# Optimization experiments

Measured on AMD Instinct MI355X. Metric: run time of the kernel, lower is better.

The kernel has to match this reference:

```python
import jax, jax.numpy as jnp
import numpy as np

T, F_IN, UNITS, N_CLASSES = 21, 126, 8, 27


def _run_lstm(seq, Wk, Wr, b):
    """Keras-style LSTM (gate order i,f,g,o). seq: (B,T,F) -> hs: (B,T,U)."""
    B = seq.shape[0]
    U = Wr.shape[0]
    # input projection for all timesteps at once: (B,T,4U)
    z_in = jnp.einsum('btf,fg->btg', seq, Wk) + b

    def step(carry, z_t):
        h, c = carry
        z = z_t + h @ Wr
        i, f, g, o = jnp.split(z, 4, axis=-1)
        i = jax.nn.sigmoid(i)
        f = jax.nn.sigmoid(f)
        g = jnp.tanh(g)
        o = jax.nn.sigmoid(o)
        c = f * c + i * g
        h = o * jnp.tanh(c)
        return (h, c), h

    h0 = jnp.zeros((B, U), seq.dtype)
    (_, _), hs = jax.lax.scan(step, (h0, h0), jnp.swapaxes(z_in, 0, 1))
    return jnp.swapaxes(hs, 0, 1)  # (B,T,U)


def setup_inputs() -> dict:
    key = jax.random.key(0)
    ks = jax.random.split(key, 6)
    B = 32768
    return {
        'x': jax.random.normal(ks[0], (B, T * F_IN), dtype=jnp.float32),
        'W1k': jax.random.normal(ks[1], (F_IN, 4 * UNITS), dtype=jnp.float32) * 0.1,
        'W1r': jax.random.normal(ks[2], (UNITS, 4 * UNITS), dtype=jnp.float32) * 0.1,
        'b1': jnp.zeros((4 * UNITS,), jnp.float32),
        'W2k': jax.random.normal(ks[3], (UNITS, 4 * UNITS), dtype=jnp.float32) * 0.1,
        'W2r': jax.random.normal(ks[4], (UNITS, 4 * UNITS), dtype=jnp.float32) * 0.1,
        'b2': jnp.zeros((4 * UNITS,), jnp.float32),
        'Wd': jax.random.normal(ks[5], (UNITS, N_CLASSES), dtype=jnp.float32) * 0.1,
        'bd': jnp.zeros((N_CLASSES,), jnp.float32),
    }


def reference(x, W1k, W1r, b1, W2k, W2r, b2, Wd, bd):
    B = x.shape[0]
    seq = x.reshape(B, T, F_IN)            # Reshape((21, 126))
    h1 = _run_lstm(seq, W1k, W1r, b1)      # LSTM(8, return_sequences=True)
    # dropout is identity at inference
    h2 = _run_lstm(h1, W2k, W2r, b2)[:, -1]  # LSTM(8) -> last step (B,8)
    return jax.nn.softmax(h2 @ Wd + bd)    # Dense(27, softmax)
```

## Files before the change

kernel.cpp:

```cpp
#include <hip/hip_runtime.h>


namespace {
constexpr int T_  = 21;
constexpr int FIN = 126;
constexpr int U_  = 8;
constexpr int NC  = 27;
constexpr int ZC  = 4 * U_;
constexpr int ROW = T_ * FIN;
constexpr size_t ZGRP = (size_t)T_ * ZC * 64;
}

__device__ __forceinline__ float sigm(float x) {
  return __builtin_amdgcn_rcpf(1.0f + __expf(-x));
}
__device__ __forceinline__ float tanh_f(float x) {
  return 1.0f - 2.0f * __builtin_amdgcn_rcpf(1.0f + __expf(2.0f * x));
}

__global__ __launch_bounds__(256) void zin_gemm(
    const float* __restrict__ X, const float* __restrict__ W1k,
    const float* __restrict__ b1, float* __restrict__ Z,
    int g0)
{
  __shared__ __align__(16) float xbuf[64 * FIN];

  const int tid = threadIdx.x;
  const int sl  = tid & 63;
  const int wv  = __builtin_amdgcn_readfirstlane(tid >> 6);
  const int grp = g0 + blockIdx.x;
  const int t   = blockIdx.y;

  const float* xbase = X + (size_t)grp * 64 * ROW + t * FIN;
  #pragma unroll
  for (int k = 0; k < 16; ++k) {
    int j = tid + k * 256;
    if (j < 64 * 63) {
      int s = j / 63;
      int q = j - s * 63;
      float2 v = *reinterpret_cast<const float2*>(xbase + (size_t)s * ROW + 2 * q);
      *reinterpret_cast<float2*>(&xbuf[s * FIN + 2 * q]) = v;
    }
  }
  __syncthreads();

  const float4* Wk4 = reinterpret_cast<const float4*>(W1k) + 2 * wv;
  float4 za = reinterpret_cast<const float4*>(b1)[2 * wv];
  float4 zb = reinterpret_cast<const float4*>(b1)[2 * wv + 1];

  const float2* xr = reinterpret_cast<const float2*>(&xbuf[sl * FIN]);
  #pragma unroll 3
  for (int q = 0; q < 63; ++q) {
    float2 xv = xr[q];
    float4 wa0 = Wk4[(2 * q) * 8];
    float4 wb0 = Wk4[(2 * q) * 8 + 1];
    float4 wa1 = Wk4[(2 * q + 1) * 8];
    float4 wb1 = Wk4[(2 * q + 1) * 8 + 1];
    za.x = fmaf(xv.x, wa0.x, za.x); za.y = fmaf(xv.x, wa0.y, za.y);
    za.z = fmaf(xv.x, wa0.z, za.z); za.w = fmaf(xv.x, wa0.w, za.w);
    zb.x = fmaf(xv.x, wb0.x, zb.x); zb.y = fmaf(xv.x, wb0.y, zb.y);
    zb.z = fmaf(xv.x, wb0.z, zb.z); zb.w = fmaf(xv.x, wb0.w, zb.w);
    za.x = fmaf(xv.y, wa1.x, za.x); za.y = fmaf(xv.y, wa1.y, za.y);
    za.z = fmaf(xv.y, wa1.z, za.z); za.w = fmaf(xv.y, wa1.w, za.w);
    zb.x = fmaf(xv.y, wb1.x, zb.x); zb.y = fmaf(xv.y, wb1.y, zb.y);
    zb.z = fmaf(xv.y, wb1.z, zb.z); zb.w = fmaf(xv.y, wb1.w, zb.w);
  }

  float* zp = Z + (size_t)(grp - g0) * ZGRP + (size_t)t * ZC * 64
            + (size_t)(8 * wv) * 64 + sl;
  zp[0 * 64] = za.x; zp[1 * 64] = za.y; zp[2 * 64] = za.z; zp[3 * 64] = za.w;
  zp[4 * 64] = zb.x; zp[5 * 64] = zb.y; zp[6 * 64] = zb.z; zp[7 * 64] = zb.w;
}

__global__ __launch_bounds__(64) void lstm_rec(
    const float* __restrict__ Z,
    const float* __restrict__ W1r,
    const float* __restrict__ W2k, const float* __restrict__ W2r,
    const float* __restrict__ b2,
    const float* __restrict__ Wd, const float* __restrict__ bd,
    float* __restrict__ out, int g0)
{
  const int sl  = threadIdx.x & 63;
  const int grp = g0 + blockIdx.x;

  const float* zb = Z + (size_t)(grp - g0) * ZGRP + sl;

  float h1[U_], c1[U_], h2[U_], c2[U_];
  #pragma unroll
  for (int u = 0; u < U_; ++u) { h1[u] = 0.f; c1[u] = 0.f; h2[u] = 0.f; c2[u] = 0.f; }

  float zc[ZC], zn[ZC];
  #pragma unroll
  for (int c = 0; c < ZC; ++c) zc[c] = zb[c * 64];

  for (int t = 0; t < T_; ++t) {
    if (t + 1 < T_) {
      const float* zt = zb + (size_t)(t + 1) * ZC * 64;
      #pragma unroll
      for (int c = 0; c < ZC; ++c) zn[c] = zt[c * 64];
    }

    float z1[ZC];
    #pragma unroll
    for (int c = 0; c < ZC; ++c) z1[c] = zc[c];
    #pragma unroll
    for (int k = 0; k < U_; ++k) {
      float hv = h1[k];
      #pragma unroll
      for (int c = 0; c < ZC; ++c) z1[c] = fmaf(hv, W1r[k * ZC + c], z1[c]);
    }
    #pragma unroll
    for (int u = 0; u < U_; ++u) {
      float iv = sigm(z1[u]), fv = sigm(z1[U_ + u]);
      float gv = tanh_f(z1[2 * U_ + u]), ov = sigm(z1[3 * U_ + u]);
      float cn = fv * c1[u] + iv * gv;
      c1[u] = cn;
      h1[u] = ov * tanh_f(cn);
    }

    float z2[ZC];
    #pragma unroll
    for (int c = 0; c < ZC; ++c) z2[c] = b2[c];
    #pragma unroll
    for (int k = 0; k < U_; ++k) {
      float hv = h1[k];
      #pragma unroll
      for (int c = 0; c < ZC; ++c) z2[c] = fmaf(hv, W2k[k * ZC + c], z2[c]);
    }
    #pragma unroll
    for (int k = 0; k < U_; ++k) {
      float hv = h2[k];
      #pragma unroll
      for (int c = 0; c < ZC; ++c) z2[c] = fmaf(hv, W2r[k * ZC + c], z2[c]);
    }
    #pragma unroll
    for (int u = 0; u < U_; ++u) {
      float iv = sigm(z2[u]), fv = sigm(z2[U_ + u]);
      float gv = tanh_f(z2[2 * U_ + u]), ov = sigm(z2[3 * U_ + u]);
      float cn = fv * c2[u] + iv * gv;
      c2[u] = cn;
      h2[u] = ov * tanh_f(cn);
    }

    #pragma unroll
    for (int c = 0; c < ZC; ++c) zc[c] = zn[c];
  }

  float lg[NC];
  float m = -1e30f;
  #pragma unroll
  for (int c = 0; c < NC; ++c) {
    float acc = bd[c];
    #pragma unroll
    for (int k = 0; k < U_; ++k) acc = fmaf(h2[k], Wd[k * NC + c], acc);
    lg[c] = acc;
    m = fmaxf(m, acc);
  }
  float ssum = 0.f;
  #pragma unroll
  for (int c = 0; c < NC; ++c) {
    float e = __expf(lg[c] - m);
    lg[c] = e;
    ssum += e;
  }
  float inv = 1.0f / ssum;
  float* op = out + (size_t)(grp * 64 + sl) * NC;
  #pragma unroll
  for (int c = 0; c < NC; ++c) op[c] = lg[c] * inv;
}

extern "C" void kernel_launch(void* const* d_in, const int* in_sizes, int n_in,
                              void* d_out, int out_size, void* d_ws, size_t ws_size,
                              hipStream_t stream) {
  const float* X   = (const float*)d_in[0];
  const float* W1k = (const float*)d_in[1];
  const float* W1r = (const float*)d_in[2];
  const float* b1  = (const float*)d_in[3];
  const float* W2k = (const float*)d_in[4];
  const float* W2r = (const float*)d_in[5];
  const float* b2  = (const float*)d_in[6];
  const float* Wd  = (const float*)d_in[7];
  const float* bd  = (const float*)d_in[8];
  float* out = (float*)d_out;
  float* Z   = (float*)d_ws;

  const int B    = in_sizes[0] / ROW;
  const int ngrp = B / 64;

  const size_t zgrp_bytes = ZGRP * sizeof(float);
  int gpc = (int)(ws_size / zgrp_bytes);
  if (gpc < 1) gpc = 1;
  if (gpc > ngrp) gpc = ngrp;

  for (int g0 = 0; g0 < ngrp; g0 += gpc) {
    int g1 = g0 + gpc;
    if (g1 > ngrp) g1 = ngrp;
    int n = g1 - g0;
    zin_gemm<<<dim3(n, T_), 256, 0, stream>>>(X, W1k, b1, Z, g0);
    lstm_rec<<<dim3(n), 64, 0, stream>>>(Z, W1r, W2k, W2r, b2, Wd, bd, out, g0);
  }
}
```

Before: 618.0 us.

## Split LSTM gate matmuls across four waves and pipeline input GEMM loads over timesteps

The recurrent kernel now runs four waves per 64-sample group. Each wave computes an 8-gate slice of the recurrent and layer-2 matmuls and exchanges pre-activations through shared memory with barriers, and the softmax output is staged in LDS for coalesced stores. The input projection kernel now loops over all 21 timesteps in one block, prefetching the next timestep's inputs into registers while it computes on a double-buffered LDS copy. This cuts per-thread serial work and register pressure in the recurrence at the cost of two barriers per step. The GEMM grid shrinks by a factor of 21, which may reduce parallelism.

```diff
diff --git a/kernel.cpp b/kernel.cpp
--- a/kernel.cpp
+++ b/kernel.cpp
@@ -23,56 +23,80 @@
     const float* __restrict__ b1, float* __restrict__ Z,
     int g0)
 {
-  __shared__ __align__(16) float xbuf[64 * FIN];
+  __shared__ __align__(16) float xb[2][64 * FIN];
 
   const int tid = threadIdx.x;
   const int sl  = tid & 63;
   const int wv  = __builtin_amdgcn_readfirstlane(tid >> 6);
   const int grp = g0 + blockIdx.x;
-  const int t   = blockIdx.y;
-
-  const float* xbase = X + (size_t)grp * 64 * ROW + t * FIN;
+
+  int  goff[16];
+  int  loff[16];
+  bool val[16];
   #pragma unroll
   for (int k = 0; k < 16; ++k) {
     int j = tid + k * 256;
-    if (j < 64 * 63) {
-      int s = j / 63;
-      int q = j - s * 63;
-      float2 v = *reinterpret_cast<const float2*>(xbase + (size_t)s * ROW + 2 * q);
-      *reinterpret_cast<float2*>(&xbuf[s * FIN + 2 * q]) = v;
-    }
-  }
-  __syncthreads();
+    val[k] = (j < 64 * 63);
+    int s = j / 63;
+    int q = j - s * 63;
+    goff[k] = s * ROW + 2 * q;
+    loff[k] = s * FIN + 2 * q;
+  }
+
+  const float* xbase = X + (size_t)grp * 64 * ROW;
 
   const float4* Wk4 = reinterpret_cast<const float4*>(W1k) + 2 * wv;
-  float4 za = reinterpret_cast<const float4*>(b1)[2 * wv];
-  float4 zb = reinterpret_cast<const float4*>(b1)[2 * wv + 1];
-
-  const float2* xr = reinterpret_cast<const float2*>(&xbuf[sl * FIN]);
-  #pragma unroll 3
-  for (int q = 0; q < 63; ++q) {
-    float2 xv = xr[q];
-    float4 wa0 = Wk4[(2 * q) * 8];
-    float4 wb0 = Wk4[(2 * q) * 8 + 1];
-    float4 wa1 = Wk4[(2 * q + 1) * 8];
-    float4 wb1 = Wk4[(2 * q + 1) * 8 + 1];
-    za.x = fmaf(xv.x, wa0.x, za.x); za.y = fmaf(xv.x, wa0.y, za.y);
-    za.z = fmaf(xv.x, wa0.z, za.z); za.w = fmaf(xv.x, wa0.w, za.w);
-    zb.x = fmaf(xv.x, wb0.x, zb.x); zb.y = fmaf(xv.x, wb0.y, zb.y);
-    zb.z = fmaf(xv.x, wb0.z, zb.z); zb.w = fmaf(xv.x, wb0.w, zb.w);
-    za.x = fmaf(xv.y, wa1.x, za.x); za.y = fmaf(xv.y, wa1.y, za.y);
-    za.z = fmaf(xv.y, wa1.z, za.z); za.w = fmaf(xv.y, wa1.w, za.w);
-    zb.x = fmaf(xv.y, wb1.x, zb.x); zb.y = fmaf(xv.y, wb1.y, zb.y);
-    zb.z = fmaf(xv.y, wb1.z, zb.z); zb.w = fmaf(xv.y, wb1.w, zb.w);
-  }
-
-  float* zp = Z + (size_t)(grp - g0) * ZGRP + (size_t)t * ZC * 64
-            + (size_t)(8 * wv) * 64 + sl;
-  zp[0 * 64] = za.x; zp[1 * 64] = za.y; zp[2 * 64] = za.z; zp[3 * 64] = za.w;
-  zp[4 * 64] = zb.x; zp[5 * 64] = zb.y; zp[6 * 64] = zb.z; zp[7 * 64] = zb.w;
-}
-
-__global__ __launch_bounds__(64) void lstm_rec(
+  const float4  b1a = reinterpret_cast<const float4*>(b1)[2 * wv];
+  const float4  b1b = reinterpret_cast<const float4*>(b1)[2 * wv + 1];
+
+  float2 pf[16];
+  #pragma unroll
+  for (int k = 0; k < 16; ++k)
+    if (val[k]) pf[k] = *reinterpret_cast<const float2*>(xbase + goff[k]);
+
+  int p = 0;
+  for (int t = 0; t < T_; ++t) {
+    #pragma unroll
+    for (int k = 0; k < 16; ++k)
+      if (val[k]) *reinterpret_cast<float2*>(&xb[p][loff[k]]) = pf[k];
+    __syncthreads();
+
+    if (t + 1 < T_) {
+      const float* xt = xbase + (t + 1) * FIN;
+      #pragma unroll
+      for (int k = 0; k < 16; ++k)
+        if (val[k]) pf[k] = *reinterpret_cast<const float2*>(xt + goff[k]);
+    }
+
+    float4 za = b1a, zb = b1b;
+    const float2* xr = reinterpret_cast<const float2*>(&xb[p][sl * FIN]);
+    #pragma unroll 3
+    for (int q = 0; q < 63; ++q) {
+      float2 xv = xr[q];
+      float4 wa0 = Wk4[(2 * q) * 8];
+      float4 wb0 = Wk4[(2 * q) * 8 + 1];
+      float4 wa1 = Wk4[(2 * q + 1) * 8];
+      float4 wb1 = Wk4[(2 * q + 1) * 8 + 1];
+      za.x = fmaf(xv.x, wa0.x, za.x); za.y = fmaf(xv.x, wa0.y, za.y);
+      za.z = fmaf(xv.x, wa0.z, za.z); za.w = fmaf(xv.x, wa0.w, za.w);
+      zb.x = fmaf(xv.x, wb0.x, zb.x); zb.y = fmaf(xv.x, wb0.y, zb.y);
+      zb.z = fmaf(xv.x, wb0.z, zb.z); zb.w = fmaf(xv.x, wb0.w, zb.w);
+      za.x = fmaf(xv.y, wa1.x, za.x); za.y = fmaf(xv.y, wa1.y, za.y);
+      za.z = fmaf(xv.y, wa1.z, za.z); za.w = fmaf(xv.y, wa1.w, za.w);
+      zb.x = fmaf(xv.y, wb1.x, zb.x); zb.y = fmaf(xv.y, wb1.y, zb.y);
+      zb.z = fmaf(xv.y, wb1.z, zb.z); zb.w = fmaf(xv.y, wb1.w, zb.w);
+    }
+
+    float* zp = Z + (size_t)(grp - g0) * ZGRP + (size_t)t * ZC * 64
+              + (size_t)(8 * wv) * 64 + sl;
+    zp[0 * 64] = za.x; zp[1 * 64] = za.y; zp[2 * 64] = za.z; zp[3 * 64] = za.w;
+    zp[4 * 64] = zb.x; zp[5 * 64] = zb.y; zp[6 * 64] = zb.z; zp[7 * 64] = zb.w;
+
+    p ^= 1;
+  }
+}
+
+__global__ __launch_bounds__(256) void lstm_rec(
     const float* __restrict__ Z,
     const float* __restrict__ W1r,
     const float* __restrict__ W2k, const float* __restrict__ W2r,
@@ -80,70 +104,99 @@
     const float* __restrict__ Wd, const float* __restrict__ bd,
     float* __restrict__ out, int g0)
 {
-  const int sl  = threadIdx.x & 63;
+  __shared__ __align__(16) float zb1[ZC * 64];
+  __shared__ __align__(16) float zb2[ZC * 64];
+
+  const int tid = threadIdx.x;
+  const int sl  = tid & 63;
+  const int wv  = __builtin_amdgcn_readfirstlane(tid >> 6);
   const int grp = g0 + blockIdx.x;
 
-  const float* zb = Z + (size_t)(grp - g0) * ZGRP + sl;
+  const float* zbase = Z + (size_t)(grp - g0) * ZGRP + (size_t)(8 * wv) * 64 + sl;
+
+  const float4 b2a = reinterpret_cast<const float4*>(b2)[2 * wv];
+  const float4 b2b = reinterpret_cast<const float4*>(b2)[2 * wv + 1];
 
   float h1[U_], c1[U_], h2[U_], c2[U_];
   #pragma unroll
   for (int u = 0; u < U_; ++u) { h1[u] = 0.f; c1[u] = 0.f; h2[u] = 0.f; c2[u] = 0.f; }
 
-  float zc[ZC], zn[ZC];
-  #pragma unroll
-  for (int c = 0; c < ZC; ++c) zc[c] = zb[c * 64];
+  float zn[8], zc[8];
+  #pragma unroll
+  for (int c = 0; c < 8; ++c) zn[c] = zbase[c * 64];
 
   for (int t = 0; t < T_; ++t) {
+    #pragma unroll
+    for (int c = 0; c < 8; ++c) zc[c] = zn[c];
     if (t + 1 < T_) {
-      const float* zt = zb + (size_t)(t + 1) * ZC * 64;
+      const float* zt = zbase + (size_t)(t + 1) * ZC * 64;
       #pragma unroll
-      for (int c = 0; c < ZC; ++c) zn[c] = zt[c * 64];
-    }
-
-    float z1[ZC];
-    #pragma unroll
-    for (int c = 0; c < ZC; ++c) z1[c] = zc[c];
+      for (int c = 0; c < 8; ++c) zn[c] = zt[c * 64];
+    }
+
+    float z1[8];
+    #pragma unroll
+    for (int c = 0; c < 8; ++c) z1[c] = zc[c];
     #pragma unroll
     for (int k = 0; k < U_; ++k) {
       float hv = h1[k];
       #pragma unroll
-      for (int c = 0; c < ZC; ++c) z1[c] = fmaf(hv, W1r[k * ZC + c], z1[c]);
-    }
+      for (int c = 0; c < 8; ++c)
+        z1[c] = fmaf(hv, W1r[k * ZC + 8 * wv + c], z1[c]);
+    }
+    #pragma unroll
+    for (int c = 0; c < 8; ++c) zb1[(8 * wv + c) * 64 + sl] = z1[c];
+    __syncthreads();
+
     #pragma unroll
     for (int u = 0; u < U_; ++u) {
-      float iv = sigm(z1[u]), fv = sigm(z1[U_ + u]);
-      float gv = tanh_f(z1[2 * U_ + u]), ov = sigm(z1[3 * U_ + u]);
+      float zi = zb1[u * 64 + sl];
+      float zf = zb1[(U_ + u) * 64 + sl];
+      float zg = zb1[(2 * U_ + u) * 64 + sl];
+      float zo = zb1[(3 * U_ + u) * 64 + sl];
+      float iv = sigm(zi), fv = sigm(zf), gv = tanh_f(zg), ov = sigm(zo);
       float cn = fv * c1[u] + iv * gv;
       c1[u] = cn;
       h1[u] = ov * tanh_f(cn);
     }
 
-    float z2[ZC];
-    #pragma unroll
-    for (int c = 0; c < ZC; ++c) z2[c] = b2[c];
+    float4 za = b2a, zbv = b2b;
     #pragma unroll
     for (int k = 0; k < U_; ++k) {
       float hv = h1[k];
-      #pragma unroll
-      for (int c = 0; c < ZC; ++c) z2[c] = fmaf(hv, W2k[k * ZC + c], z2[c]);
+      const float* w = &W2k[k * ZC + 8 * wv];
+      za.x  = fmaf(hv, w[0], za.x);  za.y  = fmaf(hv, w[1], za.y);
+      za.z  = fmaf(hv, w[2], za.z);  za.w  = fmaf(hv, w[3], za.w);
+      zbv.x = fmaf(hv, w[4], zbv.x); zbv.y = fmaf(hv, w[5], zbv.y);
+      zbv.z = fmaf(hv, w[6], zbv.z); zbv.w = fmaf(hv, w[7], zbv.w);
     }
     #pragma unroll
     for (int k = 0; k < U_; ++k) {
       float hv = h2[k];
-      #pragma unroll
-      for (int c = 0; c < ZC; ++c) z2[c] = fmaf(hv, W2r[k * ZC + c], z2[c]);
-    }
+      const float* w = &W2r[k * ZC + 8 * wv];
+      za.x  = fmaf(hv, w[0], za.x);  za.y  = fmaf(hv, w[1], za.y);
+      za.z  = fmaf(hv, w[2], za.z);  za.w  = fmaf(hv, w[3], za.w);
+      zbv.x = fmaf(hv, w[4], zbv.x); zbv.y = fmaf(hv, w[5], zbv.y);
+      zbv.z = fmaf(hv, w[6], zbv.z); zbv.w = fmaf(hv, w[7], zbv.w);
+    }
+    {
+      float* zp = &zb2[(8 * wv) * 64 + sl];
+      zp[0 * 64] = za.x;  zp[1 * 64] = za.y;  zp[2 * 64] = za.z;  zp[3 * 64] = za.w;
+      zp[4 * 64] = zbv.x; zp[5 * 64] = zbv.y; zp[6 * 64] = zbv.z; zp[7 * 64] = zbv.w;
+    }
+    __syncthreads();
+
     #pragma unroll
     for (int u = 0; u < U_; ++u) {
-      float iv = sigm(z2[u]), fv = sigm(z2[U_ + u]);
-      float gv = tanh_f(z2[2 * U_ + u]), ov = sigm(z2[3 * U_ + u]);
+      float zi = zb2[u * 64 + sl];
+      float zf = zb2[(U_ + u) * 64 + sl];
+      float zg = zb2[(2 * U_ + u) * 64 + sl];
+      float zo = zb2[(3 * U_ + u) * 64 + sl];
+      float iv = sigm(zi), fv = sigm(zf), gv = tanh_f(zg), ov = sigm(zo);
       float cn = fv * c2[u] + iv * gv;
       c2[u] = cn;
       h2[u] = ov * tanh_f(cn);
     }
-
-    #pragma unroll
-    for (int c = 0; c < ZC; ++c) zc[c] = zn[c];
   }
 
   float lg[NC];
@@ -164,9 +217,19 @@
     ssum += e;
   }
   float inv = 1.0f / ssum;
-  float* op = out + (size_t)(grp * 64 + sl) * NC;
-  #pragma unroll
-  for (int c = 0; c < NC; ++c) op[c] = lg[c] * inv;
+  if (wv == 0) {
+    #pragma unroll
+    for (int c = 0; c < NC; ++c) zb1[sl * NC + c] = lg[c] * inv;
+  }
+  __syncthreads();
+  {
+    float* oblk = out + (size_t)grp * 64 * NC;
+    #pragma unroll
+    for (int k = 0; k < 7; ++k) {
+      int j = tid + k * 256;
+      if (j < 64 * NC) oblk[j] = zb1[j];
+    }
+  }
 }
 
 extern "C" void kernel_launch(void* const* d_in, const int* in_sizes, int n_in,
@@ -196,7 +259,7 @@
     int g1 = g0 + gpc;
     if (g1 > ngrp) g1 = ngrp;
     int n = g1 - g0;
-    zin_gemm<<<dim3(n, T_), 256, 0, stream>>>(X, W1k, b1, Z, g0);
-    lstm_rec<<<dim3(n), 64, 0, stream>>>(Z, W1r, W2k, W2r, b2, Wd, bd, out, g0);
-  }
-}
+    zin_gemm<<<dim3(n), 256, 0, stream>>>(X, W1k, b1, Z, g0);
+    lstm_rec<<<dim3(n), 256, 0, stream>>>(Z, W1r, W2k, W2r, b2, Wd, bd, out, g0);
+  }
+}
```

After: 583.6 us. -5.6%, faster.
